# Optimization experiments

Measured on AMD Instinct MI355X. Metric: run time of the kernel, lower is better.

The kernel has to match this reference:

```python
import jax, jax.numpy as jnp
import numpy as np

N_ITERS = 5
BONUS = 10.0          # strict_maxima_bonus
MAX_SHIFT = 0.6       # max_subpixel_shift
RADIUS = 1            # dilation_radius
EPS = 1e-7


def setup_inputs() -> dict:
    key = jax.random.key(0)
    x = jax.random.normal(key, (2, 4, 8, 512, 512), dtype=jnp.float32)
    return {"x": x}


def _forward(x):
    B, C, D, H, W = x.shape
    dt = x.dtype
    HW, DHW = H * W, D * H * W

    # nms3d(input, (3,3,3), mask_only=True): x equals max over 3x3x3 window (-inf pad)
    mx = jax.lax.reduce_window(x, -jnp.inf, jax.lax.max,
                               (1, 1, 3, 3, 3), (1, 1, 1, 1, 1), 'SAME')
    nms = x == mx

    # shifted views: sh(ds,dh,dw)[...,d,h,w] = x[...,d+ds,h+dh,w+dw] (zero pad; only interior used)
    xp = jnp.pad(x, ((0, 0), (0, 0), (1, 1), (1, 1), (1, 1)))
    sh = lambda ds, dh, dw: xp[:, :, 1 + ds:1 + ds + D, 1 + dh:1 + dh + H, 1 + dw:1 + dw + W]

    # x = width (W axis), y = height (H axis), s = scale (D axis)
    gx = 0.5 * (sh(0, 0, 1) - sh(0, 0, -1))
    gy = 0.5 * (sh(0, 1, 0) - sh(0, -1, 0))
    gs = 0.5 * (sh(1, 0, 0) - sh(-1, 0, 0))
    dxx = sh(0, 0, 1) - 2.0 * x + sh(0, 0, -1)
    dyy = sh(0, 1, 0) - 2.0 * x + sh(0, -1, 0)
    dss = sh(1, 0, 0) - 2.0 * x + sh(-1, 0, 0)
    dxy = 0.25 * (sh(0, 1, 1) - sh(0, 1, -1) - sh(0, -1, 1) + sh(0, -1, -1))
    dxs = 0.25 * (sh(1, 0, 1) - sh(1, 0, -1) - sh(-1, 0, 1) + sh(-1, 0, -1))
    dys = 0.25 * (sh(1, 1, 0) - sh(1, -1, 0) - sh(-1, 1, 0) + sh(-1, -1, 0))

    # Cramer's rule for symmetric 3x3 H * s = -g
    r0, r1, r2 = -gx, -gy, -gs
    cf00 = dyy * dss - dys * dys
    cf01 = dxy * dss - dys * dxs
    cf02 = dxy * dys - dyy * dxs
    det = dxx * cf00 - dxy * cf01 + dxs * cf02
    sol_f = jnp.abs(det) > EPS
    sdet = jnp.where(sol_f, det, jnp.ones_like(det))
    sx_f = (r0 * cf00 - dxy * (r1 * dss - dys * r2) + dxs * (r1 * dys - dyy * r2)) / sdet
    sy_f = (dxx * (r1 * dss - dys * r2) - r0 * cf01 + dxs * (dxy * r2 - r1 * dxs)) / sdet
    ss_f = (dxx * (dyy * r2 - r1 * dys) - dxy * (dxy * r2 - r1 * dxs) + r0 * cf02) / sdet
    gds_f = gx * sx_f + gy * sy_f + gs * ss_f

    sx_fl, sy_fl, ss_fl = sx_f.reshape(-1), sy_f.reshape(-1), ss_f.reshape(-1)
    gds_fl, sol_fl = gds_f.reshape(-1), sol_f.reshape(-1)

    # dense per-voxel iteration state (only NMS maxima matter)
    gd = jnp.broadcast_to(jnp.arange(D, dtype=jnp.int32).reshape(1, 1, D, 1, 1), x.shape)
    gh = jnp.broadcast_to(jnp.arange(H, dtype=jnp.int32).reshape(1, 1, 1, H, 1), x.shape)
    gw = jnp.broadcast_to(jnp.arange(W, dtype=jnp.int32).reshape(1, 1, 1, 1, W), x.shape)
    bc_base = (jnp.arange(B * C, dtype=jnp.int32).reshape(B, C, 1, 1, 1) * DHW)

    cur_d, cur_h, cur_w = gd, gh, gw
    valid = nms
    shx = jnp.zeros_like(x); shy = jnp.zeros_like(x); shs = jnp.zeros_like(x)
    gdsv = jnp.zeros_like(x)

    for _ in range(N_ITERS):
        di = jnp.clip(cur_d, 1, D - 2)
        hi = jnp.clip(cur_h, 1, H - 2)
        wi = jnp.clip(cur_w, 1, W - 2)
        idx = bc_base + di * HW + hi * W + wi
        valid = valid & sol_fl[idx]
        vf = valid
        shx = jnp.where(vf, sx_fl[idx], 0.0)
        shy = jnp.where(vf, sy_fl[idx], 0.0)
        shs = jnp.where(vf, ss_fl[idx], 0.0)
        gdsv = jnp.where(vf, gds_fl[idx], 0.0)
        # move integer centre one step along any axis whose shift exceeds threshold
        mvw = jnp.where(jnp.abs(shx) > MAX_SHIFT, jnp.sign(shx), 0.0).astype(jnp.int32)
        mvh = jnp.where(jnp.abs(shy) > MAX_SHIFT, jnp.sign(shy), 0.0).astype(jnp.int32)
        mvd = jnp.where(jnp.abs(shs) > MAX_SHIFT, jnp.sign(shs), 0.0).astype(jnp.int32)
        cur_w = cur_w + mvw
        cur_h = cur_h + mvh
        cur_d = cur_d + mvd
        # keypoints leaving the precomputed L-inf ball are invalid
        valid = valid & (jnp.abs(cur_d - gd) <= RADIUS) \
                      & (jnp.abs(cur_h - gh) <= RADIUS) \
                      & (jnp.abs(cur_w - gw) <= RADIUS)

    use = nms & valid
    coord_s = jnp.where(use, cur_d.astype(dt) + shs, gd.astype(dt))
    coord_x = jnp.where(use, cur_w.astype(dt) + shx, gw.astype(dt))
    coord_y = jnp.where(use, cur_h.astype(dt) + shy, gh.astype(dt))
    coords_max = jnp.stack([coord_s, coord_x, coord_y], axis=2)  # (B,C,3,D,H,W)
    y_max = x + jnp.where(use, 0.5 * gdsv, 0.0) + BONUS * nms.astype(dt)
    return coords_max, y_max


def reference(x):
    return _forward(x)
```

## Files before the change

kernel.cpp:

```cpp
#include <hip/hip_runtime.h>

#define DD 8
#define HH 512
#define WW 512
#define HW (HH * WW)
#define DHW (DD * HW)
#define BC 8
#define NITERS 5
#define TCAP 512u

typedef float vf4 __attribute__((ext_vector_type(4)));

__device__ __forceinline__ float max3f(float a, float b, float c) {
    return fmaxf(fmaxf(a, b), c);
}

__device__ __forceinline__ bool solve_at(const float* __restrict__ xb,
                                         int di, int hi, int wi,
                                         float& sx, float& sy, float& ss, float& gds)
{
    const float* p = xb + (size_t)di * HW + (size_t)hi * WW + wi;
    float v   = p[0];
    float xpw = p[1],        xmw = p[-1];
    float xph = p[WW],       xmh = p[-WW];
    float xpd = p[HW],       xmd = p[-HW];
    float g1  = p[WW + 1],   g2  = p[WW - 1],   g3 = p[-WW + 1],  g4 = p[-WW - 1];
    float h1  = p[HW + 1],   h2  = p[HW - 1],   h3 = p[-HW + 1],  h4 = p[-HW - 1];
    float i1  = p[HW + WW],  i2  = p[HW - WW],  i3 = p[-HW + WW], i4 = p[-HW - WW];

    float gx = 0.5f * (xpw - xmw);
    float gy = 0.5f * (xph - xmh);
    float gs = 0.5f * (xpd - xmd);
    float dxx = xpw + xmw - 2.0f * v;
    float dyy = xph + xmh - 2.0f * v;
    float dss = xpd + xmd - 2.0f * v;
    float dxy = 0.25f * (g1 - g2 - g3 + g4);
    float dxs = 0.25f * (h1 - h2 - h3 + h4);
    float dys = 0.25f * (i1 - i2 - i3 + i4);

    float r0 = -gx, r1 = -gy, r2 = -gs;
    float cf00 = dyy * dss - dys * dys;
    float cf01 = dxy * dss - dys * dxs;
    float cf02 = dxy * dys - dyy * dxs;
    float det  = dxx * cf00 - dxy * cf01 + dxs * cf02;
    if (!(fabsf(det) > 1e-7f)) return false;

    float t0 = r1 * dss - dys * r2;
    float t1 = r1 * dys - dyy * r2;
    float t2 = dxy * r2 - r1 * dxs;
    float t3 = dyy * r2 - r1 * dys;
    sx = (r0 * cf00 - dxy * t0 + dxs * t1) / det;
    sy = (dxx * t0 - r0 * cf01 + dxs * t2) / det;
    ss = (dxx * t3 - dxy * t2 + r0 * cf02) / det;
    gds = gx * sx + gy * sy + gs * ss;
    return true;
}

#define COMPUTE(d, M, CEN) {                                                               \
    const float* s  = xb + (size_t)(d) * HW;                                               \
    const float* r0 = s + (size_t)hm * WW;                                                 \
    const float* r1 = s + (size_t)h  * WW;                                                 \
    const float* r2 = s + (size_t)hp * WW;                                                 \
    vf4 va = *(const vf4*)(r0 + w0);                                                       \
    float  la = r0[w0 ? w0 - 1 : 0], ra = r0[w0 < 508 ? w0 + 4 : 511];                     \
    vf4 vb = *(const vf4*)(r1 + w0);                                                       \
    float  lb = r1[w0 ? w0 - 1 : 0], rb = r1[w0 < 508 ? w0 + 4 : 511];                     \
    vf4 vc = *(const vf4*)(r2 + w0);                                                       \
    float  lc = r2[w0 ? w0 - 1 : 0], rc = r2[w0 < 508 ? w0 + 4 : 511];                     \
    (M).x = max3f(max3f(la, va.x, va.y), max3f(lb, vb.x, vb.y), max3f(lc, vc.x, vc.y));    \
    (M).y = max3f(max3f(va.x, va.y, va.z), max3f(vb.x, vb.y, vb.z), max3f(vc.x, vc.y, vc.z)); \
    (M).z = max3f(max3f(va.y, va.z, va.w), max3f(vb.y, vb.z, vb.w), max3f(vc.y, vc.z, vc.w)); \
    (M).w = max3f(max3f(va.z, va.w, ra), max3f(vb.z, vb.w, rb), max3f(vc.z, vc.w, rc));    \
    (CEN) = vb; }

#define FLAG(d, MP, MC, MN) {                                                              \
    float mx0 = max3f((MP).x, (MC).x, (MN).x);                                             \
    float mx1 = max3f((MP).y, (MC).y, (MN).y);                                             \
    float mx2 = max3f((MP).z, (MC).z, (MN).z);                                             \
    float mx3 = max3f((MP).w, (MC).w, (MN).w);                                             \
    bool n0 = cen[d].x == mx0, n1 = cen[d].y == mx1, n2 = cen[d].z == mx2, n3 = cen[d].w == mx3; \
    nmsmask |= ((n0?1u:0u)|(n1?2u:0u)|(n2?4u:0u)|(n3?8u:0u)) << (4*(d));                   \
    unsigned long long b0 = __ballot(n0), b1 = __ballot(n1), b2 = __ballot(n2), b3 = __ballot(n3); \
    unsigned tot = (unsigned)(__popcll(b0) + __popcll(b1) + __popcll(b2) + __popcll(b3));  \
    unsigned base = 0;                                                                     \
    if (tot) {                                                                             \
        if (lane == 0) base = atomicAdd(&ls_count, tot);                                   \
        base = (unsigned)__shfl((int)base, 0, 64);                                         \
        unsigned long long below = ((unsigned long long)1 << lane) - 1;                    \
        unsigned vix = (unsigned)(((d) * 2 + rrow) * WW + w0);                             \
        unsigned o = base, p;                                                              \
        p = o + (unsigned)__popcll(b0 & below); if (n0 && p < TCAP) ls_list[p] = (unsigned short)vix;       \
        o += (unsigned)__popcll(b0);                                                       \
        p = o + (unsigned)__popcll(b1 & below); if (n1 && p < TCAP) ls_list[p] = (unsigned short)(vix + 1); \
        o += (unsigned)__popcll(b1);                                                       \
        p = o + (unsigned)__popcll(b2 & below); if (n2 && p < TCAP) ls_list[p] = (unsigned short)(vix + 2); \
        o += (unsigned)__popcll(b2);                                                       \
        p = o + (unsigned)__popcll(b3 & below); if (n3 && p < TCAP) ls_list[p] = (unsigned short)(vix + 3); \
    }                                                                                      \
    if (lane == 0) ls_wbase[wid * 8 + (d)] = (unsigned short)base; }

__global__ __launch_bounds__(256) void fused10_kernel(const float* __restrict__ x,
                                                      float* __restrict__ out)
{
    __shared__ unsigned ls_count;
    __shared__ unsigned short ls_list[TCAP];
    __shared__ unsigned short ls_wbase[4 * 8];
    __shared__ vf4 ls_tab[TCAP];

    if (threadIdx.x == 0) ls_count = 0;
    __syncthreads();

    int b = (blockIdx.x & 7) * 256 + (blockIdx.x >> 3);
    int tid = b * 256 + threadIdx.x;
    int w4 = tid & 127;
    int h  = (tid >> 7) & 511;
    int bc = tid >> 16;
    int w0 = w4 << 2;
    int lane = threadIdx.x & 63;
    int wid  = threadIdx.x >> 6;
    int rrow = threadIdx.x >> 7;
    int h0blk = h - rrow;

    const float* xb = x + (size_t)bc * DHW;
    float* ybase = out + (size_t)(BC * 3) * DHW;
    int hm = h ? h - 1 : 0, hp = h < 511 ? h + 1 : 511;

    vf4 cen[DD];
    unsigned nmsmask = 0;
    vf4 m0, m1, m2r;
    COMPUTE(0, m0, cen[0]);
    COMPUTE(1, m1, cen[1]);
    FLAG(0, m0, m0, m1);
    COMPUTE(2, m2r, cen[2]);
    FLAG(1, m0, m1, m2r);
    COMPUTE(3, m0, cen[3]);
    FLAG(2, m1, m2r, m0);
    COMPUTE(4, m1, cen[4]);
    FLAG(3, m2r, m0, m1);
    COMPUTE(5, m2r, cen[5]);
    FLAG(4, m0, m1, m2r);
    COMPUTE(6, m0, cen[6]);
    FLAG(5, m1, m2r, m0);
    COMPUTE(7, m1, cen[7]);
    FLAG(6, m2r, m0, m1);
    FLAG(7, m0, m1, m1);

    __syncthreads();
    unsigned n = ls_count;
    if (n > TCAP) n = TCAP;

    for (unsigned i = threadIdx.x; i < n; i += 256) {
        unsigned v = ls_list[i];
        int rw = v & 511;
        int rr = (v >> 9) & 1;
        int rd = v >> 10;
        int rh = h0blk + rr;

        int cd = rd, ch = rh, cw = rw;
        bool valid = true;
        float shx = 0.f, shy = 0.f, shs = 0.f, gds = 0.f;
        for (int it = 0; it < NITERS; ++it) {
            int di = cd < 1 ? 1 : (cd > DD - 2 ? DD - 2 : cd);
            int hi = ch < 1 ? 1 : (ch > HH - 2 ? HH - 2 : ch);
            int wi = cw < 1 ? 1 : (cw > WW - 2 ? WW - 2 : cw);
            float sx, sy, ss, g;
            if (!solve_at(xb, di, hi, wi, sx, sy, ss, g)) { valid = false; break; }
            shx = sx; shy = sy; shs = ss; gds = g;
            int mvw = (fabsf(sx) > 0.6f) ? (sx > 0.f ? 1 : -1) : 0;
            int mvh = (fabsf(sy) > 0.6f) ? (sy > 0.f ? 1 : -1) : 0;
            int mvd = (fabsf(ss) > 0.6f) ? (ss > 0.f ? 1 : -1) : 0;
            if ((mvw | mvh | mvd) == 0) break;
            cw += mvw; ch += mvh; cd += mvd;
            int ad = cd - rd; if (ad < 0) ad = -ad;
            int ah = ch - rh; if (ah < 0) ah = -ah;
            int aw = cw - rw; if (aw < 0) aw = -aw;
            if (ad > 1 || ah > 1 || aw > 1) { valid = false; break; }
        }
        vf4 t;
        if (valid) {
            t.x = (float)cd + shs; t.y = (float)cw + shx;
            t.z = (float)ch + shy; t.w = 0.5f * gds;
        } else {
            t.x = (float)rd; t.y = (float)rw; t.z = (float)rh; t.w = 0.0f;
        }
        ls_tab[i] = t;
    }

    __syncthreads();

    #pragma unroll
    for (int d = 0; d < DD; ++d) {
        unsigned fl = (nmsmask >> (4 * d)) & 15u;
        bool n0 = fl & 1u, n1 = fl & 2u, n2 = fl & 4u, n3 = fl & 8u;
        vf4 csv = { (float)d, (float)d, (float)d, (float)d };
        vf4 cxv = { (float)w0, (float)(w0 + 1), (float)(w0 + 2), (float)(w0 + 3) };
        vf4 cyv = { (float)h, (float)h, (float)h, (float)h };
        vf4 yv  = { cen[d].x + (n0 ? 10.0f : 0.0f),
                    cen[d].y + (n1 ? 10.0f : 0.0f),
                    cen[d].z + (n2 ? 10.0f : 0.0f),
                    cen[d].w + (n3 ? 10.0f : 0.0f) };
        unsigned long long b0 = __ballot(n0), b1 = __ballot(n1), b2 = __ballot(n2), b3 = __ballot(n3);
        if (fl) {
            unsigned long long below = ((unsigned long long)1 << lane) - 1;
            unsigned basew = ls_wbase[wid * 8 + d];
            unsigned c0 = (unsigned)__popcll(b0), c1 = (unsigned)__popcll(b1), c2 = (unsigned)__popcll(b2);
            unsigned p0 = basew + (unsigned)__popcll(b0 & below);
            unsigned p1 = basew + c0 + (unsigned)__popcll(b1 & below);
            unsigned p2 = basew + c0 + c1 + (unsigned)__popcll(b2 & below);
            unsigned p3 = basew + c0 + c1 + c2 + (unsigned)__popcll(b3 & below);
            if (n0 && p0 < TCAP) { vf4 t = ls_tab[p0]; csv.x = t.x; cxv.x = t.y; cyv.x = t.z; yv.x += t.w; }
            if (n1 && p1 < TCAP) { vf4 t = ls_tab[p1]; csv.y = t.x; cxv.y = t.y; cyv.y = t.z; yv.y += t.w; }
            if (n2 && p2 < TCAP) { vf4 t = ls_tab[p2]; csv.z = t.x; cxv.z = t.y; cyv.z = t.z; yv.z += t.w; }
            if (n3 && p3 < TCAP) { vf4 t = ls_tab[p3]; csv.w = t.x; cxv.w = t.y; cyv.w = t.z; yv.w += t.w; }
        }
        size_t rowoff = (size_t)d * HW + (size_t)h * WW + w0;
        __builtin_nontemporal_store(csv, (vf4*)(out + ((size_t)bc * 3 + 0) * DHW + rowoff));
        __builtin_nontemporal_store(cxv, (vf4*)(out + ((size_t)bc * 3 + 1) * DHW + rowoff));
        __builtin_nontemporal_store(cyv, (vf4*)(out + ((size_t)bc * 3 + 2) * DHW + rowoff));
        __builtin_nontemporal_store(yv,  (vf4*)(ybase + (size_t)bc * DHW + rowoff));
    }
}

extern "C" void kernel_launch(void* const* d_in, const int* in_sizes, int n_in,
                              void* d_out, int out_size, void* d_ws, size_t ws_size,
                              hipStream_t stream)
{
    const float* x = (const float*)d_in[0];
    float* out = (float*)d_out;
    int total = BC * HH * (WW / 4);
    hipLaunchKernelGGL(fused10_kernel, dim3(total / 256), dim3(256), 0, stream, x, out);
}
```

Measured before the change: 83.90 us.

## Split depth processing into two half-depth passes per block with alternating order

Each block now handles the 8 depth slices in two passes of 4: it computes NMS flags, refines keypoints and stores outputs for one half, then does the same for the other half. Odd blocks take the halves in reverse order so neighbouring blocks are in different phases. The aim is to interleave the store-heavy phase with the load and compute phase across blocks, and to shrink register state (4 centre rows instead of 8). The cost is one extra boundary slice loaded per pass, more barriers, and a second shared-list cycle per block.

```diff
diff --git a/kernel.cpp b/kernel.cpp
--- a/kernel.cpp
+++ b/kernel.cpp
@@ -73,13 +73,13 @@
     (M).w = max3f(max3f(va.z, va.w, ra), max3f(vb.z, vb.w, rb), max3f(vc.z, vc.w, rc));    \
     (CEN) = vb; }
 
-#define FLAG(d, MP, MC, MN) {                                                              \
+#define FLAGP(d, di, MP, MC, MN, CEN) {                                                    \
     float mx0 = max3f((MP).x, (MC).x, (MN).x);                                             \
     float mx1 = max3f((MP).y, (MC).y, (MN).y);                                             \
     float mx2 = max3f((MP).z, (MC).z, (MN).z);                                             \
     float mx3 = max3f((MP).w, (MC).w, (MN).w);                                             \
-    bool n0 = cen[d].x == mx0, n1 = cen[d].y == mx1, n2 = cen[d].z == mx2, n3 = cen[d].w == mx3; \
-    nmsmask |= ((n0?1u:0u)|(n1?2u:0u)|(n2?4u:0u)|(n3?8u:0u)) << (4*(d));                   \
+    bool n0 = (CEN).x == mx0, n1 = (CEN).y == mx1, n2 = (CEN).z == mx2, n3 = (CEN).w == mx3; \
+    nmsmask |= ((n0?1u:0u)|(n1?2u:0u)|(n2?4u:0u)|(n3?8u:0u)) << (4*(di));                  \
     unsigned long long b0 = __ballot(n0), b1 = __ballot(n1), b2 = __ballot(n2), b3 = __ballot(n3); \
     unsigned tot = (unsigned)(__popcll(b0) + __popcll(b1) + __popcll(b2) + __popcll(b3));  \
     unsigned base = 0;                                                                     \
@@ -97,18 +97,15 @@
         o += (unsigned)__popcll(b2);                                                       \
         p = o + (unsigned)__popcll(b3 & below); if (n3 && p < TCAP) ls_list[p] = (unsigned short)(vix + 3); \
     }                                                                                      \
-    if (lane == 0) ls_wbase[wid * 8 + (d)] = (unsigned short)base; }
-
-__global__ __launch_bounds__(256) void fused10_kernel(const float* __restrict__ x,
+    if (lane == 0) ls_wbase[wid * 4 + (di)] = (unsigned short)base; }
+
+__global__ __launch_bounds__(256) void fused12_kernel(const float* __restrict__ x,
                                                       float* __restrict__ out)
 {
     __shared__ unsigned ls_count;
     __shared__ unsigned short ls_list[TCAP];
-    __shared__ unsigned short ls_wbase[4 * 8];
+    __shared__ unsigned short ls_wbase[4 * 4];
     __shared__ vf4 ls_tab[TCAP];
-
-    if (threadIdx.x == 0) ls_count = 0;
-    __syncthreads();
 
     int b = (blockIdx.x & 7) * 256 + (blockIdx.x >> 3);
     int tid = b * 256 + threadIdx.x;
@@ -125,99 +122,114 @@
     float* ybase = out + (size_t)(BC * 3) * DHW;
     int hm = h ? h - 1 : 0, hp = h < 511 ? h + 1 : 511;
 
-    vf4 cen[DD];
-    unsigned nmsmask = 0;
-    vf4 m0, m1, m2r;
-    COMPUTE(0, m0, cen[0]);
-    COMPUTE(1, m1, cen[1]);
-    FLAG(0, m0, m0, m1);
-    COMPUTE(2, m2r, cen[2]);
-    FLAG(1, m0, m1, m2r);
-    COMPUTE(3, m0, cen[3]);
-    FLAG(2, m1, m2r, m0);
-    COMPUTE(4, m1, cen[4]);
-    FLAG(3, m2r, m0, m1);
-    COMPUTE(5, m2r, cen[5]);
-    FLAG(4, m0, m1, m2r);
-    COMPUTE(6, m0, cen[6]);
-    FLAG(5, m1, m2r, m0);
-    COMPUTE(7, m1, cen[7]);
-    FLAG(6, m2r, m0, m1);
-    FLAG(7, m0, m1, m1);
-
-    __syncthreads();
-    unsigned n = ls_count;
-    if (n > TCAP) n = TCAP;
-
-    for (unsigned i = threadIdx.x; i < n; i += 256) {
-        unsigned v = ls_list[i];
-        int rw = v & 511;
-        int rr = (v >> 9) & 1;
-        int rd = v >> 10;
-        int rh = h0blk + rr;
-
-        int cd = rd, ch = rh, cw = rw;
-        bool valid = true;
-        float shx = 0.f, shy = 0.f, shs = 0.f, gds = 0.f;
-        for (int it = 0; it < NITERS; ++it) {
-            int di = cd < 1 ? 1 : (cd > DD - 2 ? DD - 2 : cd);
-            int hi = ch < 1 ? 1 : (ch > HH - 2 ? HH - 2 : ch);
-            int wi = cw < 1 ? 1 : (cw > WW - 2 ? WW - 2 : cw);
-            float sx, sy, ss, g;
-            if (!solve_at(xb, di, hi, wi, sx, sy, ss, g)) { valid = false; break; }
-            shx = sx; shy = sy; shs = ss; gds = g;
-            int mvw = (fabsf(sx) > 0.6f) ? (sx > 0.f ? 1 : -1) : 0;
-            int mvh = (fabsf(sy) > 0.6f) ? (sy > 0.f ? 1 : -1) : 0;
-            int mvd = (fabsf(ss) > 0.6f) ? (ss > 0.f ? 1 : -1) : 0;
-            if ((mvw | mvh | mvd) == 0) break;
-            cw += mvw; ch += mvh; cd += mvd;
-            int ad = cd - rd; if (ad < 0) ad = -ad;
-            int ah = ch - rh; if (ah < 0) ah = -ah;
-            int aw = cw - rw; if (aw < 0) aw = -aw;
-            if (ad > 1 || ah > 1 || aw > 1) { valid = false; break; }
+    for (int pass = 0; pass < 2; ++pass) {
+        int dlo = ((b & 1) ? (1 - pass) : pass) * 4;
+
+        __syncthreads();
+        if (threadIdx.x == 0) ls_count = 0;
+        __syncthreads();
+
+        unsigned nmsmask = 0;
+        vf4 m[5];
+        vf4 cen[4];
+        vf4 dump;
+        if (dlo == 0) {
+            COMPUTE(0, m[0], cen[0]);
+            COMPUTE(1, m[1], cen[1]);
+            COMPUTE(2, m[2], cen[2]);
+            COMPUTE(3, m[3], cen[3]);
+            COMPUTE(4, m[4], dump);
+            FLAGP(0, 0, m[0], m[0], m[1], cen[0]);
+            FLAGP(1, 1, m[0], m[1], m[2], cen[1]);
+            FLAGP(2, 2, m[1], m[2], m[3], cen[2]);
+            FLAGP(3, 3, m[2], m[3], m[4], cen[3]);
+        } else {
+            COMPUTE(3, m[0], dump);
+            COMPUTE(4, m[1], cen[0]);
+            COMPUTE(5, m[2], cen[1]);
+            COMPUTE(6, m[3], cen[2]);
+            COMPUTE(7, m[4], cen[3]);
+            FLAGP(4, 0, m[0], m[1], m[2], cen[0]);
+            FLAGP(5, 1, m[1], m[2], m[3], cen[1]);
+            FLAGP(6, 2, m[2], m[3], m[4], cen[2]);
+            FLAGP(7, 3, m[3], m[4], m[4], cen[3]);
         }
-        vf4 t;
-        if (valid) {
-            t.x = (float)cd + shs; t.y = (float)cw + shx;
-            t.z = (float)ch + shy; t.w = 0.5f * gds;
-        } else {
-            t.x = (float)rd; t.y = (float)rw; t.z = (float)rh; t.w = 0.0f;
+
+        __syncthreads();
+        unsigned n = ls_count;
+        if (n > TCAP) n = TCAP;
+
+        for (unsigned i = threadIdx.x; i < n; i += 256) {
+            unsigned v = ls_list[i];
+            int rw = v & 511;
+            int rr = (v >> 9) & 1;
+            int rd = v >> 10;
+            int rh = h0blk + rr;
+
+            int cd = rd, ch = rh, cw = rw;
+            bool valid = true;
+            float shx = 0.f, shy = 0.f, shs = 0.f, gds = 0.f;
+            for (int it = 0; it < NITERS; ++it) {
+                int di = cd < 1 ? 1 : (cd > DD - 2 ? DD - 2 : cd);
+                int hi = ch < 1 ? 1 : (ch > HH - 2 ? HH - 2 : ch);
+                int wi = cw < 1 ? 1 : (cw > WW - 2 ? WW - 2 : cw);
+                float sx, sy, ss, g;
+                if (!solve_at(xb, di, hi, wi, sx, sy, ss, g)) { valid = false; break; }
+                shx = sx; shy = sy; shs = ss; gds = g;
+                int mvw = (fabsf(sx) > 0.6f) ? (sx > 0.f ? 1 : -1) : 0;
+                int mvh = (fabsf(sy) > 0.6f) ? (sy > 0.f ? 1 : -1) : 0;
+                int mvd = (fabsf(ss) > 0.6f) ? (ss > 0.f ? 1 : -1) : 0;
+                if ((mvw | mvh | mvd) == 0) break;
+                cw += mvw; ch += mvh; cd += mvd;
+                int ad = cd - rd; if (ad < 0) ad = -ad;
+                int ah = ch - rh; if (ah < 0) ah = -ah;
+                int aw = cw - rw; if (aw < 0) aw = -aw;
+                if (ad > 1 || ah > 1 || aw > 1) { valid = false; break; }
+            }
+            vf4 t;
+            if (valid) {
+                t.x = (float)cd + shs; t.y = (float)cw + shx;
+                t.z = (float)ch + shy; t.w = 0.5f * gds;
+            } else {
+                t.x = (float)rd; t.y = (float)rw; t.z = (float)rh; t.w = 0.0f;
+            }
+            ls_tab[i] = t;
         }
-        ls_tab[i] = t;
-    }
-
-    __syncthreads();
-
-    #pragma unroll
-    for (int d = 0; d < DD; ++d) {
-        unsigned fl = (nmsmask >> (4 * d)) & 15u;
-        bool n0 = fl & 1u, n1 = fl & 2u, n2 = fl & 4u, n3 = fl & 8u;
-        vf4 csv = { (float)d, (float)d, (float)d, (float)d };
-        vf4 cxv = { (float)w0, (float)(w0 + 1), (float)(w0 + 2), (float)(w0 + 3) };
-        vf4 cyv = { (float)h, (float)h, (float)h, (float)h };
-        vf4 yv  = { cen[d].x + (n0 ? 10.0f : 0.0f),
-                    cen[d].y + (n1 ? 10.0f : 0.0f),
-                    cen[d].z + (n2 ? 10.0f : 0.0f),
-                    cen[d].w + (n3 ? 10.0f : 0.0f) };
-        unsigned long long b0 = __ballot(n0), b1 = __ballot(n1), b2 = __ballot(n2), b3 = __ballot(n3);
-        if (fl) {
-            unsigned long long below = ((unsigned long long)1 << lane) - 1;
-            unsigned basew = ls_wbase[wid * 8 + d];
-            unsigned c0 = (unsigned)__popcll(b0), c1 = (unsigned)__popcll(b1), c2 = (unsigned)__popcll(b2);
-            unsigned p0 = basew + (unsigned)__popcll(b0 & below);
-            unsigned p1 = basew + c0 + (unsigned)__popcll(b1 & below);
-            unsigned p2 = basew + c0 + c1 + (unsigned)__popcll(b2 & below);
-            unsigned p3 = basew + c0 + c1 + c2 + (unsigned)__popcll(b3 & below);
-            if (n0 && p0 < TCAP) { vf4 t = ls_tab[p0]; csv.x = t.x; cxv.x = t.y; cyv.x = t.z; yv.x += t.w; }
-            if (n1 && p1 < TCAP) { vf4 t = ls_tab[p1]; csv.y = t.x; cxv.y = t.y; cyv.y = t.z; yv.y += t.w; }
-            if (n2 && p2 < TCAP) { vf4 t = ls_tab[p2]; csv.z = t.x; cxv.z = t.y; cyv.z = t.z; yv.z += t.w; }
-            if (n3 && p3 < TCAP) { vf4 t = ls_tab[p3]; csv.w = t.x; cxv.w = t.y; cyv.w = t.z; yv.w += t.w; }
+
+        __syncthreads();
+
+        #pragma unroll
+        for (int di = 0; di < 4; ++di) {
+            int d = dlo + di;
+            unsigned fl = (nmsmask >> (4 * di)) & 15u;
+            bool n0 = fl & 1u, n1 = fl & 2u, n2 = fl & 4u, n3 = fl & 8u;
+            vf4 csv = { (float)d, (float)d, (float)d, (float)d };
+            vf4 cxv = { (float)w0, (float)(w0 + 1), (float)(w0 + 2), (float)(w0 + 3) };
+            vf4 cyv = { (float)h, (float)h, (float)h, (float)h };
+            vf4 yv  = { cen[di].x + (n0 ? 10.0f : 0.0f),
+                        cen[di].y + (n1 ? 10.0f : 0.0f),
+                        cen[di].z + (n2 ? 10.0f : 0.0f),
+                        cen[di].w + (n3 ? 10.0f : 0.0f) };
+            unsigned long long b0 = __ballot(n0), b1 = __ballot(n1), b2 = __ballot(n2), b3 = __ballot(n3);
+            if (fl) {
+                unsigned long long below = ((unsigned long long)1 << lane) - 1;
+                unsigned basew = ls_wbase[wid * 4 + di];
+                unsigned c0 = (unsigned)__popcll(b0), c1 = (unsigned)__popcll(b1), c2 = (unsigned)__popcll(b2);
+                unsigned p0 = basew + (unsigned)__popcll(b0 & below);
+                unsigned p1 = basew + c0 + (unsigned)__popcll(b1 & below);
+                unsigned p2 = basew + c0 + c1 + (unsigned)__popcll(b2 & below);
+                unsigned p3 = basew + c0 + c1 + c2 + (unsigned)__popcll(b3 & below);
+                if (n0 && p0 < TCAP) { vf4 t = ls_tab[p0]; csv.x = t.x; cxv.x = t.y; cyv.x = t.z; yv.x += t.w; }
+                if (n1 && p1 < TCAP) { vf4 t = ls_tab[p1]; csv.y = t.x; cxv.y = t.y; cyv.y = t.z; yv.y += t.w; }
+                if (n2 && p2 < TCAP) { vf4 t = ls_tab[p2]; csv.z = t.x; cxv.z = t.y; cyv.z = t.z; yv.z += t.w; }
+                if (n3 && p3 < TCAP) { vf4 t = ls_tab[p3]; csv.w = t.x; cxv.w = t.y; cyv.w = t.z; yv.w += t.w; }
+            }
+            size_t rowoff = (size_t)d * HW + (size_t)h * WW + w0;
+            __builtin_nontemporal_store(csv, (vf4*)(out + ((size_t)bc * 3 + 0) * DHW + rowoff));
+            __builtin_nontemporal_store(cxv, (vf4*)(out + ((size_t)bc * 3 + 1) * DHW + rowoff));
+            __builtin_nontemporal_store(cyv, (vf4*)(out + ((size_t)bc * 3 + 2) * DHW + rowoff));
+            __builtin_nontemporal_store(yv,  (vf4*)(ybase + (size_t)bc * DHW + rowoff));
         }
-        size_t rowoff = (size_t)d * HW + (size_t)h * WW + w0;
-        __builtin_nontemporal_store(csv, (vf4*)(out + ((size_t)bc * 3 + 0) * DHW + rowoff));
-        __builtin_nontemporal_store(cxv, (vf4*)(out + ((size_t)bc * 3 + 1) * DHW + rowoff));
-        __builtin_nontemporal_store(cyv, (vf4*)(out + ((size_t)bc * 3 + 2) * DHW + rowoff));
-        __builtin_nontemporal_store(yv,  (vf4*)(ybase + (size_t)bc * DHW + rowoff));
     }
 }
 
@@ -228,5 +240,5 @@
     const float* x = (const float*)d_in[0];
     float* out = (float*)d_out;
     int total = BC * HH * (WW / 4);
-    hipLaunchKernelGGL(fused10_kernel, dim3(total / 256), dim3(256), 0, stream, x, out);
-}
+    hipLaunchKernelGGL(fused12_kernel, dim3(total / 256), dim3(256), 0, stream, x, out);
+}
```

New measurement: 98.15 us. +17.0%, slower.
